# Optimization experiments

Hardware: AMD Instinct MI355X
Metric: run time of the kernel (lower is better)

## Reference

```python
import jax, jax.numpy as jnp
import numpy as np

E = 400000          # total child edges in the ready batch
P = 100000          # number of parent nodes (segments)
D = 256             # 2 * model_dim


def setup_inputs() -> dict:
    key = jax.random.key(0)
    ks = jax.random.split(key, 6)
    child_hs = jax.random.normal(ks[0], (E, D), dtype=jnp.float32)
    child_cs = jax.random.normal(ks[1], (E, D), dtype=jnp.float32)
    segment_ids = jnp.sort(jax.random.randint(ks[2], (E,), 0, P))
    W_gates = jax.random.normal(ks[3], (D, 3 * D), dtype=jnp.float32) * (1.0 / np.sqrt(D))
    b_gates = jnp.zeros((3 * D,), dtype=jnp.float32)
    W_f = jax.random.normal(ks[4], (D, D), dtype=jnp.float32) * (1.0 / np.sqrt(D))
    b_f = jnp.zeros((D,), dtype=jnp.float32)
    return {
        "child_hs": child_hs,
        "child_cs": child_cs,
        "segment_ids": segment_ids,
        "num_segments": P,
        "W_gates": W_gates,
        "b_gates": b_gates,
        "W_f": W_f,
        "b_f": b_f,
    }


def reference(child_hs, child_cs, segment_ids, num_segments, W_gates, b_gates, W_f, b_f):
    # child_hs_sum per parent (segment reduce over children)
    hs_sum = jax.ops.segment_sum(child_hs, segment_ids, num_segments=num_segments)  # [P, D]
    # gates = Linear(2*model_dim -> 6*model_dim), chunk into i, o, g
    gates = hs_sum @ W_gates + b_gates                         # [P, 3D]
    i, o, g = jnp.split(gates, 3, axis=1)
    i, o, g = jax.nn.sigmoid(i), jax.nn.sigmoid(o), jnp.tanh(g)
    # per-child forget gates, fc = f * c, segment-reduced per parent
    f = jax.nn.sigmoid(child_hs @ W_f + b_f)                   # [E, D]
    fc = jax.ops.segment_sum(f * child_cs, segment_ids, num_segments=num_segments)  # [P, D]
    # child-sum LSTM update
    c = i * g + fc
    h = o * jnp.tanh(c)
    return h, c
```

## Files before the change

### kernel.cpp

```cpp
#include <hip/hip_runtime.h>
#include <hip/hip_bf16.h>

typedef __attribute__((ext_vector_type(8))) short short8;
typedef __attribute__((ext_vector_type(4))) float floatx4;

#define DD 256
#define PPB 32
#define FSTRIDE 264

__device__ __forceinline__ unsigned short f2bf(float f) {
    unsigned int u = __builtin_bit_cast(unsigned int, f);
    u += 0x7FFFu + ((u >> 16) & 1u);
    return (unsigned short)(u >> 16);
}

__device__ __forceinline__ float sigm(float x) { return 1.0f / (1.0f + __expf(-x)); }
__device__ __forceinline__ float tanh_fast(float x) { return 2.0f / (1.0f + __expf(-2.0f * x)) - 1.0f; }

__device__ __forceinline__ short8 pack8(float4 a, float4 b) {
    short8 r;
    r[0] = (short)f2bf(a.x); r[1] = (short)f2bf(a.y);
    r[2] = (short)f2bf(a.z); r[3] = (short)f2bf(a.w);
    r[4] = (short)f2bf(b.x); r[5] = (short)f2bf(b.y);
    r[6] = (short)f2bf(b.z); r[7] = (short)f2bf(b.w);
    return r;
}

__device__ __forceinline__ void stage16(const unsigned short* g, unsigned short* l) {
    __builtin_amdgcn_global_load_lds(
        (const __attribute__((address_space(1))) unsigned int*)g,
        (__attribute__((address_space(3))) unsigned int*)l, 16, 0, 0);
}

__global__ void pack_weights(const float* __restrict__ W_f, const float* __restrict__ W_g,
                             unsigned short* __restrict__ WfT, unsigned short* __restrict__ WgT) {
    int idx = blockIdx.x * 256 + threadIdx.x;
    if (idx < 65536) {
        int n = idx >> 8, k = idx & 255;
        WfT[idx] = f2bf(W_f[k * 256 + n]);
    } else {
        int i2 = idx - 65536;
        int n = i2 >> 8, k = i2 & 255;
        WgT[i2] = f2bf(W_g[k * 768 + n]);
    }
}

__global__ void build_start(const int* __restrict__ seg, int E, int P, int* __restrict__ start) {
    int e = blockIdx.x * blockDim.x + threadIdx.x;
    if (e >= E) return;
    int s = seg[e];
    if (e == 0) {
        for (int p = 0; p <= s; ++p) start[p] = 0;
    } else {
        int sp = seg[e - 1];
        for (int p = sp + 1; p <= s; ++p) start[p] = e;
    }
    if (e == E - 1) {
        for (int p = s + 1; p <= P; ++p) start[p] = E;
    }
}

__global__ void hs_reduce(const float* __restrict__ child_hs, const int* __restrict__ start,
                          int P, float* __restrict__ hs_sum) {
    int wave = threadIdx.x >> 6, lane = threadIdx.x & 63;
    int p = blockIdx.x * 4 + wave;
    if (p >= P) return;
    int lo = start[p], hi = start[p + 1];
    float4 acc = make_float4(0.f, 0.f, 0.f, 0.f);
    const float4* src = (const float4*)child_hs;
    int e = lo;
    for (; e + 4 <= hi; e += 4) {
        float4 v0 = src[(size_t)(e + 0) * 64 + lane];
        float4 v1 = src[(size_t)(e + 1) * 64 + lane];
        float4 v2 = src[(size_t)(e + 2) * 64 + lane];
        float4 v3 = src[(size_t)(e + 3) * 64 + lane];
        acc.x += v0.x + v1.x + v2.x + v3.x;
        acc.y += v0.y + v1.y + v2.y + v3.y;
        acc.z += v0.z + v1.z + v2.z + v3.z;
        acc.w += v0.w + v1.w + v2.w + v3.w;
    }
    for (; e < hi; ++e) {
        float4 v = src[(size_t)e * 64 + lane];
        acc.x += v.x; acc.y += v.y; acc.z += v.z; acc.w += v.w;
    }
    ((float4*)hs_sum)[(size_t)p * 64 + lane] = acc;
}

__global__ __launch_bounds__(256, 2) void gemm1_fc(
    const float* __restrict__ child_hs, const float* __restrict__ child_cs,
    const int* __restrict__ seg, const int* __restrict__ start,
    const unsigned short* __restrict__ WfT, const float* __restrict__ b_f,
    float* __restrict__ fc, int E, int P) {
    __shared__ __align__(16) unsigned short ldsB[8192];
    __shared__ __align__(16) float fcacc[PPB * FSTRIDE];
    const int tid = threadIdx.x;
    const int w = tid >> 6, lane = tid & 63;
    const int nl = lane & 15, q = lane >> 4;
    const int p0 = blockIdx.x * PPB;
    const int lo = start[p0], hi = start[p0 + PPB];

    for (int i = tid; i < PPB * FSTRIDE / 4; i += 256)
        ((float4*)fcacc)[i] = make_float4(0.f, 0.f, 0.f, 0.f);

    const unsigned short* Wsrc = WfT + ((w * 64 + nl) << 8) + q * 8;

    for (int cb = lo; cb < hi; cb += 64) {
        floatx4 acc[16];
#pragma unroll
        for (int t = 0; t < 16; ++t) acc[t] = (floatx4){0.f, 0.f, 0.f, 0.f};

        int erow = cb + w * 16 + nl;
        const float* Arow = child_hs + (size_t)(erow < E ? erow : E - 1) * DD + q * 8;

        for (int ks = 0; ks < 8; ++ks) {
            __syncthreads();
#pragma unroll
            for (int r = 0; r < 4; ++r)
                stage16(Wsrc + ks * 32 + (r << 12), &ldsB[(w * 4 + r) << 9]);
            float4 a0 = *(const float4*)(Arow + ks * 32);
            float4 a1 = *(const float4*)(Arow + ks * 32 + 4);
            short8 af = pack8(a0, a1);
            __syncthreads();
#pragma unroll
            for (int t = 0; t < 16; ++t) {
                short8 bf = ((const short8*)ldsB)[t * 64 + lane];
                acc[t] = __builtin_amdgcn_mfma_f32_16x16x32_bf16(af, bf, acc[t], 0, 0, 0);
            }
        }

        int e0 = cb + w * 16 + q * 4;
        int sr[4];
#pragma unroll
        for (int r = 0; r < 4; ++r) {
            int e = e0 + r;
            sr[r] = (e < hi) ? (seg[e] - p0) : -1;
        }
#pragma unroll
        for (int t = 0; t < 16; ++t) {
            int n = t * 16 + nl;
            float bias = b_f[n];
            float vr[4];
#pragma unroll
            for (int r = 0; r < 4; ++r) {
                float cs = (sr[r] >= 0) ? child_cs[(size_t)(e0 + r) * DD + n] : 0.f;
                vr[r] = sigm(acc[t][r] + bias) * cs;
            }
            float a = vr[0]; int s = sr[0];
#pragma unroll
            for (int r = 1; r < 4; ++r) {
                if (sr[r] == s) { a += vr[r]; }
                else {
                    if (s >= 0) atomicAdd(&fcacc[s * FSTRIDE + n], a);
                    a = vr[r]; s = sr[r];
                }
            }
            if (s >= 0) atomicAdd(&fcacc[s * FSTRIDE + n], a);
        }
    }

    __syncthreads();
    for (int i = tid; i < PPB * 64; i += 256) {
        int row = i >> 6, c4 = i & 63;
        float4 v = *(const float4*)&fcacc[row * FSTRIDE + c4 * 4];
        ((float4*)fc)[(((size_t)(p0 + row)) << 6) + c4] = v;
    }
}

__global__ __launch_bounds__(512, 2) void gemm2_lstm(
    const float* __restrict__ hs_sum, const unsigned short* __restrict__ WgT,
    const float* __restrict__ b_g, float* __restrict__ h_out, float* __restrict__ c_out, int P) {
    __shared__ __align__(16) unsigned short ldsB[24576];
    const int tid = threadIdx.x;
    const int w = tid >> 6, lane = tid & 63;
    const int wr = w >> 2, wc = w & 3;
    const int nl = lane & 15, q = lane >> 4;
    const int p_base = blockIdx.x * 64;

    floatx4 acc[2][12];
#pragma unroll
    for (int rt = 0; rt < 2; ++rt)
#pragma unroll
        for (int t = 0; t < 12; ++t) acc[rt][t] = (floatx4){0.f, 0.f, 0.f, 0.f};

    const float* Arow0 = hs_sum + (size_t)(p_base + wr * 32 + nl) * DD + q * 8;
    const float* Arow1 = Arow0 + (size_t)16 * DD;
    const unsigned short* Wsrc = WgT + ((w * 96 + nl) << 8) + q * 8;

#pragma unroll
    for (int r = 0; r < 6; ++r)
        stage16(Wsrc + (r << 12), &ldsB[(w * 6 + r) << 9]);

    for (int ks = 0; ks < 8; ++ks) {
        float4 a0 = *(const float4*)(Arow0 + ks * 32);
        float4 a1 = *(const float4*)(Arow0 + ks * 32 + 4);
        float4 a2 = *(const float4*)(Arow1 + ks * 32);
        float4 a3 = *(const float4*)(Arow1 + ks * 32 + 4);
        short8 af0 = pack8(a0, a1);
        short8 af1 = pack8(a2, a3);
        __syncthreads();
#pragma unroll
        for (int cgl = 0; cgl < 4; ++cgl) {
#pragma unroll
            for (int part = 0; part < 3; ++part) {
                int t = part * 16 + (wc * 4 + cgl);
                short8 bf = ((const short8*)ldsB)[t * 64 + lane];
                acc[0][cgl * 3 + part] =
                    __builtin_amdgcn_mfma_f32_16x16x32_bf16(af0, bf, acc[0][cgl * 3 + part], 0, 0, 0);
                acc[1][cgl * 3 + part] =
                    __builtin_amdgcn_mfma_f32_16x16x32_bf16(af1, bf, acc[1][cgl * 3 + part], 0, 0, 0);
            }
        }
        __syncthreads();
        if (ks < 7) {
            const unsigned short* ws = Wsrc + (ks + 1) * 32;
#pragma unroll
            for (int r = 0; r < 6; ++r)
                stage16(ws + (r << 12), &ldsB[(w * 6 + r) << 9]);
        }
    }

#pragma unroll
    for (int rt = 0; rt < 2; ++rt) {
#pragma unroll
        for (int cgl = 0; cgl < 4; ++cgl) {
            int n = (wc * 4 + cgl) * 16 + nl;
            float bi = b_g[n], bo = b_g[256 + n], bg = b_g[512 + n];
#pragma unroll
            for (int reg = 0; reg < 4; ++reg) {
                int p = p_base + wr * 32 + rt * 16 + q * 4 + reg;
                if (p < P) {
                    float I = acc[rt][cgl * 3 + 0][reg] + bi;
                    float O = acc[rt][cgl * 3 + 1][reg] + bo;
                    float G = acc[rt][cgl * 3 + 2][reg] + bg;
                    float iv = sigm(I), ov = sigm(O), gv = tanh_fast(G);
                    float c = iv * gv + c_out[(size_t)p * DD + n];
                    float hv = ov * tanh_fast(c);
                    h_out[(size_t)p * DD + n] = hv;
                    c_out[(size_t)p * DD + n] = c;
                }
            }
        }
    }
}

extern "C" void kernel_launch(void* const* d_in, const int* in_sizes, int n_in,
                              void* d_out, int out_size, void* d_ws, size_t ws_size,
                              hipStream_t stream) {
    const float* child_hs = (const float*)d_in[0];
    const float* child_cs = (const float*)d_in[1];
    const int*   seg      = (const int*)d_in[2];
    const float* W_gates  = (const float*)d_in[4];
    const float* b_gates  = (const float*)d_in[5];
    const float* W_f      = (const float*)d_in[6];
    const float* b_f      = (const float*)d_in[7];

    const int D = 256;
    const int E = in_sizes[0] / D;
    const int P = out_size / (2 * D);

    float* h_out = (float*)d_out;
    float* c_out = (float*)d_out + (size_t)P * D;

    unsigned short* WfT = (unsigned short*)d_ws;
    unsigned short* WgT = WfT + 65536;
    int* start = (int*)(WgT + 196608);

    pack_weights<<<1024, 256, 0, stream>>>(W_f, W_gates, WfT, WgT);
    build_start<<<(E + 255) / 256, 256, 0, stream>>>(seg, E, P, start);
    hs_reduce<<<(P + 3) / 4, 256, 0, stream>>>(child_hs, start, P, h_out);
    gemm1_fc<<<P / PPB, 256, 0, stream>>>(child_hs, child_cs, seg, start, WfT, b_f, c_out, E, P);
    gemm2_lstm<<<(P + 63) / 64, 512, 0, stream>>>(h_out, WgT, b_gates, h_out, c_out, P);
}
```

Measured before the change: 1.483 ms.

## Fuse segment reduce, forget-gate GEMM and gate GEMM into one kernel

```diff
diff --git a/kernel.cpp b/kernel.cpp
--- a/kernel.cpp
+++ b/kernel.cpp
@@ -2,11 +2,13 @@
 #include <hip/hip_bf16.h>
 
 typedef __attribute__((ext_vector_type(8))) short short8;
+typedef __attribute__((ext_vector_type(4))) short sh4;
 typedef __attribute__((ext_vector_type(4))) float floatx4;
 
 #define DD 256
 #define PPB 32
 #define FSTRIDE 264
+#define HSTRIDE 264
 
 __device__ __forceinline__ unsigned short f2bf(float f) {
     unsigned int u = __builtin_bit_cast(unsigned int, f);
@@ -60,39 +62,15 @@
     }
 }
 
-__global__ void hs_reduce(const float* __restrict__ child_hs, const int* __restrict__ start,
-                          int P, float* __restrict__ hs_sum) {
-    int wave = threadIdx.x >> 6, lane = threadIdx.x & 63;
-    int p = blockIdx.x * 4 + wave;
-    if (p >= P) return;
-    int lo = start[p], hi = start[p + 1];
-    float4 acc = make_float4(0.f, 0.f, 0.f, 0.f);
-    const float4* src = (const float4*)child_hs;
-    int e = lo;
-    for (; e + 4 <= hi; e += 4) {
-        float4 v0 = src[(size_t)(e + 0) * 64 + lane];
-        float4 v1 = src[(size_t)(e + 1) * 64 + lane];
-        float4 v2 = src[(size_t)(e + 2) * 64 + lane];
-        float4 v3 = src[(size_t)(e + 3) * 64 + lane];
-        acc.x += v0.x + v1.x + v2.x + v3.x;
-        acc.y += v0.y + v1.y + v2.y + v3.y;
-        acc.z += v0.z + v1.z + v2.z + v3.z;
-        acc.w += v0.w + v1.w + v2.w + v3.w;
-    }
-    for (; e < hi; ++e) {
-        float4 v = src[(size_t)e * 64 + lane];
-        acc.x += v.x; acc.y += v.y; acc.z += v.z; acc.w += v.w;
-    }
-    ((float4*)hs_sum)[(size_t)p * 64 + lane] = acc;
-}
-
-__global__ __launch_bounds__(256, 2) void gemm1_fc(
+__global__ __launch_bounds__(256, 2) void fused(
     const float* __restrict__ child_hs, const float* __restrict__ child_cs,
     const int* __restrict__ seg, const int* __restrict__ start,
-    const unsigned short* __restrict__ WfT, const float* __restrict__ b_f,
-    float* __restrict__ fc, int E, int P) {
+    const unsigned short* __restrict__ WfT, const unsigned short* __restrict__ WgT,
+    const float* __restrict__ b_f, const float* __restrict__ b_g,
+    float* __restrict__ h_out, float* __restrict__ c_out, int E) {
     __shared__ __align__(16) unsigned short ldsB[8192];
     __shared__ __align__(16) float fcacc[PPB * FSTRIDE];
+    __shared__ __align__(16) unsigned short hsacc[PPB * HSTRIDE];
     const int tid = threadIdx.x;
     const int w = tid >> 6, lane = tid & 63;
     const int nl = lane & 15, q = lane >> 4;
@@ -102,33 +80,25 @@
     for (int i = tid; i < PPB * FSTRIDE / 4; i += 256)
         ((float4*)fcacc)[i] = make_float4(0.f, 0.f, 0.f, 0.f);
 
-    const unsigned short* Wsrc = WfT + ((w * 64 + nl) << 8) + q * 8;
-
-    for (int cb = lo; cb < hi; cb += 64) {
-        floatx4 acc[16];
-#pragma unroll
-        for (int t = 0; t < 16; ++t) acc[t] = (floatx4){0.f, 0.f, 0.f, 0.f};
-
-        int erow = cb + w * 16 + nl;
-        const float* Arow = child_hs + (size_t)(erow < E ? erow : E - 1) * DD + q * 8;
-
-        for (int ks = 0; ks < 8; ++ks) {
-            __syncthreads();
-#pragma unroll
-            for (int r = 0; r < 4; ++r)
-                stage16(Wsrc + ks * 32 + (r << 12), &ldsB[(w * 4 + r) << 9]);
-            float4 a0 = *(const float4*)(Arow + ks * 32);
-            float4 a1 = *(const float4*)(Arow + ks * 32 + 4);
-            short8 af = pack8(a0, a1);
-            __syncthreads();
-#pragma unroll
-            for (int t = 0; t < 16; ++t) {
-                short8 bf = ((const short8*)ldsB)[t * 64 + lane];
-                acc[t] = __builtin_amdgcn_mfma_f32_16x16x32_bf16(af, bf, acc[t], 0, 0, 0);
-            }
-        }
-
-        int e0 = cb + w * 16 + q * 4;
+    for (int j = 0; j < 8; ++j) {
+        int ppl = w * 8 + j;
+        int lp = start[p0 + ppl], hp = start[p0 + ppl + 1];
+        float4 a = make_float4(0.f, 0.f, 0.f, 0.f);
+        const float4* src = (const float4*)child_hs;
+        for (int e = lp; e < hp; ++e) {
+            float4 v = src[(size_t)e * 64 + lane];
+            a.x += v.x; a.y += v.y; a.z += v.z; a.w += v.w;
+        }
+        sh4 s4;
+        s4[0] = (short)f2bf(a.x); s4[1] = (short)f2bf(a.y);
+        s4[2] = (short)f2bf(a.z); s4[3] = (short)f2bf(a.w);
+        *(sh4*)&hsacc[ppl * HSTRIDE + lane * 4] = s4;
+    }
+
+    const unsigned short* WfS = WfT + ((w * 64 + nl) << 8) + q * 8;
+
+    auto fc_epi = [&](const floatx4 (&acc)[16], int ebase) {
+        int e0 = ebase + w * 16 + q * 4;
         int sr[4];
 #pragma unroll
         for (int r = 0; r < 4; ++r) {
@@ -156,88 +126,100 @@
             }
             if (s >= 0) atomicAdd(&fcacc[s * FSTRIDE + n], a);
         }
+    };
+
+    for (int cb = lo; cb < hi; cb += 128) {
+        const bool two = (cb + 64) < hi;
+        floatx4 acc0[16], acc1[16];
+#pragma unroll
+        for (int t = 0; t < 16; ++t) {
+            acc0[t] = (floatx4){0.f, 0.f, 0.f, 0.f};
+            acc1[t] = (floatx4){0.f, 0.f, 0.f, 0.f};
+        }
+        int er0 = cb + w * 16 + nl, er1 = er0 + 64;
+        const float* A0 = child_hs + (size_t)(er0 < E ? er0 : E - 1) * DD + q * 8;
+        const float* A1 = child_hs + (size_t)(er1 < E ? er1 : E - 1) * DD + q * 8;
+
+        for (int ks = 0; ks < 8; ++ks) {
+            __syncthreads();
+#pragma unroll
+            for (int r = 0; r < 4; ++r)
+                stage16(WfS + ks * 32 + (r << 12), &ldsB[(w * 4 + r) << 9]);
+            float4 a0 = *(const float4*)(A0 + ks * 32);
+            float4 a1 = *(const float4*)(A0 + ks * 32 + 4);
+            short8 af0 = pack8(a0, a1);
+            float4 b0 = *(const float4*)(A1 + ks * 32);
+            float4 b1 = *(const float4*)(A1 + ks * 32 + 4);
+            short8 af1 = pack8(b0, b1);
+            __syncthreads();
+            if (two) {
+#pragma unroll
+                for (int t = 0; t < 16; ++t) {
+                    short8 bf = ((const short8*)ldsB)[t * 64 + lane];
+                    acc0[t] = __builtin_amdgcn_mfma_f32_16x16x32_bf16(af0, bf, acc0[t], 0, 0, 0);
+                    acc1[t] = __builtin_amdgcn_mfma_f32_16x16x32_bf16(af1, bf, acc1[t], 0, 0, 0);
+                }
+            } else {
+#pragma unroll
+                for (int t = 0; t < 16; ++t) {
+                    short8 bf = ((const short8*)ldsB)[t * 64 + lane];
+                    acc0[t] = __builtin_amdgcn_mfma_f32_16x16x32_bf16(af0, bf, acc0[t], 0, 0, 0);
+                }
+            }
+        }
+        fc_epi(acc0, cb);
+        if (two) fc_epi(acc1, cb + 64);
     }
 
     __syncthreads();
-    for (int i = tid; i < PPB * 64; i += 256) {
-        int row = i >> 6, c4 = i & 63;
-        float4 v = *(const float4*)&fcacc[row * FSTRIDE + c4 * 4];
-        ((float4*)fc)[(((size_t)(p0 + row)) << 6) + c4] = v;
-    }
-}
-
-__global__ __launch_bounds__(512, 2) void gemm2_lstm(
-    const float* __restrict__ hs_sum, const unsigned short* __restrict__ WgT,
-    const float* __restrict__ b_g, float* __restrict__ h_out, float* __restrict__ c_out, int P) {
-    __shared__ __align__(16) unsigned short ldsB[24576];
-    const int tid = threadIdx.x;
-    const int w = tid >> 6, lane = tid & 63;
-    const int wr = w >> 2, wc = w & 3;
-    const int nl = lane & 15, q = lane >> 4;
-    const int p_base = blockIdx.x * 64;
-
-    floatx4 acc[2][12];
+
+    floatx4 gacc[2][12];
 #pragma unroll
     for (int rt = 0; rt < 2; ++rt)
 #pragma unroll
-        for (int t = 0; t < 12; ++t) acc[rt][t] = (floatx4){0.f, 0.f, 0.f, 0.f};
-
-    const float* Arow0 = hs_sum + (size_t)(p_base + wr * 32 + nl) * DD + q * 8;
-    const float* Arow1 = Arow0 + (size_t)16 * DD;
-    const unsigned short* Wsrc = WgT + ((w * 96 + nl) << 8) + q * 8;
-
-#pragma unroll
-    for (int r = 0; r < 6; ++r)
-        stage16(Wsrc + (r << 12), &ldsB[(w * 6 + r) << 9]);
+        for (int t = 0; t < 12; ++t) gacc[rt][t] = (floatx4){0.f, 0.f, 0.f, 0.f};
+
+    const unsigned short* WgS = WgT + ((w * 64 + nl) << 8) + q * 8;
 
     for (int ks = 0; ks < 8; ++ks) {
-        float4 a0 = *(const float4*)(Arow0 + ks * 32);
-        float4 a1 = *(const float4*)(Arow0 + ks * 32 + 4);
-        float4 a2 = *(const float4*)(Arow1 + ks * 32);
-        float4 a3 = *(const float4*)(Arow1 + ks * 32 + 4);
-        short8 af0 = pack8(a0, a1);
-        short8 af1 = pack8(a2, a3);
-        __syncthreads();
-#pragma unroll
-        for (int cgl = 0; cgl < 4; ++cgl) {
-#pragma unroll
-            for (int part = 0; part < 3; ++part) {
-                int t = part * 16 + (wc * 4 + cgl);
-                short8 bf = ((const short8*)ldsB)[t * 64 + lane];
-                acc[0][cgl * 3 + part] =
-                    __builtin_amdgcn_mfma_f32_16x16x32_bf16(af0, bf, acc[0][cgl * 3 + part], 0, 0, 0);
-                acc[1][cgl * 3 + part] =
-                    __builtin_amdgcn_mfma_f32_16x16x32_bf16(af1, bf, acc[1][cgl * 3 + part], 0, 0, 0);
-            }
-        }
-        __syncthreads();
-        if (ks < 7) {
-            const unsigned short* ws = Wsrc + (ks + 1) * 32;
-#pragma unroll
-            for (int r = 0; r < 6; ++r)
-                stage16(ws + (r << 12), &ldsB[(w * 6 + r) << 9]);
-        }
-    }
-
-#pragma unroll
-    for (int rt = 0; rt < 2; ++rt) {
-#pragma unroll
-        for (int cgl = 0; cgl < 4; ++cgl) {
-            int n = (wc * 4 + cgl) * 16 + nl;
-            float bi = b_g[n], bo = b_g[256 + n], bg = b_g[512 + n];
+        short8 af0 = *(const short8*)&hsacc[nl * HSTRIDE + ks * 32 + q * 8];
+        short8 af1 = *(const short8*)&hsacc[(16 + nl) * HSTRIDE + ks * 32 + q * 8];
+#pragma unroll
+        for (int part = 0; part < 3; ++part) {
+            __syncthreads();
+#pragma unroll
+            for (int r = 0; r < 4; ++r)
+                stage16(WgS + part * 65536 + ks * 32 + (r << 12), &ldsB[(w * 4 + r) << 9]);
+            __syncthreads();
+#pragma unroll
+            for (int cgl = 0; cgl < 4; ++cgl) {
+                short8 bf = ((const short8*)ldsB)[(w * 4 + cgl) * 64 + lane];
+                gacc[0][cgl * 3 + part] =
+                    __builtin_amdgcn_mfma_f32_16x16x32_bf16(af0, bf, gacc[0][cgl * 3 + part], 0, 0, 0);
+                gacc[1][cgl * 3 + part] =
+                    __builtin_amdgcn_mfma_f32_16x16x32_bf16(af1, bf, gacc[1][cgl * 3 + part], 0, 0, 0);
+            }
+        }
+    }
+
+#pragma unroll
+    for (int cgl = 0; cgl < 4; ++cgl) {
+        int n = (w * 4 + cgl) * 16 + nl;
+        float bi = b_g[n], bo = b_g[256 + n], bg = b_g[512 + n];
+#pragma unroll
+        for (int rt = 0; rt < 2; ++rt) {
 #pragma unroll
             for (int reg = 0; reg < 4; ++reg) {
-                int p = p_base + wr * 32 + rt * 16 + q * 4 + reg;
-                if (p < P) {
-                    float I = acc[rt][cgl * 3 + 0][reg] + bi;
-                    float O = acc[rt][cgl * 3 + 1][reg] + bo;
-                    float G = acc[rt][cgl * 3 + 2][reg] + bg;
-                    float iv = sigm(I), ov = sigm(O), gv = tanh_fast(G);
-                    float c = iv * gv + c_out[(size_t)p * DD + n];
-                    float hv = ov * tanh_fast(c);
-                    h_out[(size_t)p * DD + n] = hv;
-                    c_out[(size_t)p * DD + n] = c;
-                }
+                int pl = rt * 16 + q * 4 + reg;
+                float I = gacc[rt][cgl * 3 + 0][reg] + bi;
+                float O = gacc[rt][cgl * 3 + 1][reg] + bo;
+                float G = gacc[rt][cgl * 3 + 2][reg] + bg;
+                float iv = sigm(I), ov = sigm(O), gv = tanh_fast(G);
+                float c = iv * gv + fcacc[pl * FSTRIDE + n];
+                float hv = ov * tanh_fast(c);
+                size_t p = (size_t)(p0 + pl);
+                h_out[p * DD + n] = hv;
+                c_out[p * DD + n] = c;
             }
         }
     }
@@ -267,7 +249,6 @@
 
     pack_weights<<<1024, 256, 0, stream>>>(W_f, W_gates, WfT, WgT);
     build_start<<<(E + 255) / 256, 256, 0, stream>>>(seg, E, P, start);
-    hs_reduce<<<(P + 3) / 4, 256, 0, stream>>>(child_hs, start, P, h_out);
-    gemm1_fc<<<P / PPB, 256, 0, stream>>>(child_hs, child_cs, seg, start, WfT, b_f, c_out, E, P);
-    gemm2_lstm<<<(P + 63) / 64, 512, 0, stream>>>(h_out, WgT, b_gates, h_out, c_out, P);
-}
+    fused<<<P / PPB, 256, 0, stream>>>(child_hs, child_cs, seg, start, WfT, WgT,
+                                       b_f, b_gates, h_out, c_out, E);
+}
```

New measurement: 1.397 ms. 5.8% less time.
